# Kernel optimization log

Hardware: AMD Instinct MI355X
Metric: run time of the kernel (lower is better)

The kernel has to match this reference:

```python
import jax, jax.numpy as jnp
import numpy as np

K = 20
EPS = 1e-5


def _knn_idx(pts, k):
    # pts: [B,N,C] -> [B,N,k] indices of k nearest neighbors (self included),
    # matching torch topk on negative squared distance.
    inner = jnp.einsum('bnc,bmc->bnm', pts, pts)
    sq = jnp.sum(pts * pts, axis=-1)
    neg_dist = 2.0 * inner - sq[:, :, None] - sq[:, None, :]  # [B,N,N]
    return jax.lax.top_k(neg_dist, k)[1]


def _graph_feature(pts, k):
    # pts: [B,N,C] -> edge features [B,N,k,2C] = concat(neighbor-center, center)
    idx = _knn_idx(pts, k)                       # [B,N,k]
    nb = jax.vmap(lambda p, i: p[i])(pts, idx)   # gather: [B,N,k,C]
    ctr = jnp.broadcast_to(pts[:, :, None, :], nb.shape)
    return jnp.concatenate([nb - ctr, ctr], axis=-1)


def _bn(x, g, b, axes):
    # BatchNorm with batch statistics (torch training-mode forward)
    m = jnp.mean(x, axes, keepdims=True)
    v = jnp.var(x, axes, keepdims=True)
    return (x - m) * jax.lax.rsqrt(v + EPS) * g + b


def _edge_block(pts, W, b, g, beta):
    # EdgeConv: graph feature -> 1x1 conv (matmul over channels) -> BN -> ReLU -> max over k
    f = _graph_feature(pts, K)                       # [B,N,k,2C]
    h = jnp.einsum('bnkc,oc->bnko', f, W) + b        # 1x1 conv
    h = jax.nn.relu(_bn(h, g, beta, (0, 1, 2)))
    return jnp.max(h, axis=2)                        # [B,N,O]


def _forward(x, conv1_w, conv1_b, bn1_g, bn1_b, conv2_w, conv2_b, bn2_g, bn2_b,
             conv3_w, conv3_b, bn3_g, bn3_b, conv4_w, conv4_b, bn4_g, bn4_b,
             fc1_w, fc1_b, bnf1_g, bnf1_b, fc2_w, fc2_b, bnf2_g, bnf2_b,
             fc3_w, fc3_b, bnf3_g, bnf3_b, fc4_w, fc4_b):
    pts = x[:, 0]  # squeeze(1): [B,N,3] (channels-last == torch [B,3,N] transposed)
    x1 = _edge_block(pts, conv1_w, conv1_b, bn1_g, bn1_b)   # [B,N,64]
    x2 = _edge_block(x1, conv2_w, conv2_b, bn2_g, bn2_b)    # [B,N,64]
    x3 = _edge_block(x2, conv3_w, conv3_b, bn3_g, bn3_b)    # [B,N,128]
    x4 = _edge_block(x3, conv4_w, conv4_b, bn4_g, bn4_b)    # [B,N,256]
    # maxpool over all N points (kernel (crop_point_num,1))
    x_64 = jnp.max(x2, axis=1)    # [B,64]
    x_128 = jnp.max(x3, axis=1)   # [B,128]
    x_256 = jnp.max(x4, axis=1)   # [B,256]
    h = jnp.concatenate([x_256, x_128, x_64], axis=1)  # [B,448]
    h = jax.nn.relu(_bn(h @ fc1_w.T + fc1_b, bnf1_g, bnf1_b, (0,)))
    h = jax.nn.relu(_bn(h @ fc2_w.T + fc2_b, bnf2_g, bnf2_b, (0,)))
    h = jax.nn.relu(_bn(h @ fc3_w.T + fc3_b, bnf3_g, bnf3_b, (0,)))
    return h @ fc4_w.T + fc4_b    # [B,1]


def setup_inputs() -> dict:
    key = jax.random.key(0)
    ks = jax.random.split(key, 16)
    B, N = 8, 2048
    f32 = jnp.float32

    def w(k, shape):
        return jax.random.normal(k, shape, f32) / np.float32(np.sqrt(shape[-1]))

    def bn_params(c):
        return jnp.ones((c,), f32), jnp.zeros((c,), f32)

    bn1_g, bn1_b = bn_params(64)
    bn2_g, bn2_b = bn_params(64)
    bn3_g, bn3_b = bn_params(128)
    bn4_g, bn4_b = bn_params(256)
    bnf1_g, bnf1_b = bn_params(256)
    bnf2_g, bnf2_b = bn_params(128)
    bnf3_g, bnf3_b = bn_params(16)
    return {
        'x': jax.random.normal(ks[0], (B, 1, N, 3), f32),
        'conv1_w': w(ks[1], (64, 6)),   'conv1_b': jnp.zeros((64,), f32),
        'bn1_g': bn1_g, 'bn1_b': bn1_b,
        'conv2_w': w(ks[2], (64, 128)), 'conv2_b': jnp.zeros((64,), f32),
        'bn2_g': bn2_g, 'bn2_b': bn2_b,
        'conv3_w': w(ks[3], (128, 128)), 'conv3_b': jnp.zeros((128,), f32),
        'bn3_g': bn3_g, 'bn3_b': bn3_b,
        'conv4_w': w(ks[4], (256, 256)), 'conv4_b': jnp.zeros((256,), f32),
        'bn4_g': bn4_g, 'bn4_b': bn4_b,
        'fc1_w': w(ks[5], (256, 448)), 'fc1_b': jnp.zeros((256,), f32),
        'bnf1_g': bnf1_g, 'bnf1_b': bnf1_b,
        'fc2_w': w(ks[6], (128, 256)), 'fc2_b': jnp.zeros((128,), f32),
        'bnf2_g': bnf2_g, 'bnf2_b': bnf2_b,
        'fc3_w': w(ks[7], (16, 128)), 'fc3_b': jnp.zeros((16,), f32),
        'bnf3_g': bnf3_g, 'bnf3_b': bnf3_b,
        'fc4_w': w(ks[8], (1, 16)), 'fc4_b': jnp.zeros((1,), f32),
    }


def reference(x, conv1_w, conv1_b, bn1_g, bn1_b, conv2_w, conv2_b, bn2_g, bn2_b,
              conv3_w, conv3_b, bn3_g, bn3_b, conv4_w, conv4_b, bn4_g, bn4_b,
              fc1_w, fc1_b, bnf1_g, bnf1_b, fc2_w, fc2_b, bnf2_g, bnf2_b,
              fc3_w, fc3_b, bnf3_g, bnf3_b, fc4_w, fc4_b):
    return _forward(x, conv1_w, conv1_b, bn1_g, bn1_b, conv2_w, conv2_b, bn2_g, bn2_b,
                    conv3_w, conv3_b, bn3_g, bn3_b, conv4_w, conv4_b, bn4_g, bn4_b,
                    fc1_w, fc1_b, bnf1_g, bnf1_b, fc2_w, fc2_b, bnf2_g, bnf2_b,
                    fc3_w, fc3_b, bnf3_g, bnf3_b, fc4_w, fc4_b)
```

## Files before the change

kernel.cpp:

```cpp
#include <hip/hip_runtime.h>
#include <hip/hip_bf16.h>
#include <cfloat>

constexpr int BATCH = 8, NPTS = 2048, KNN = 20;
constexpr int NROWS = BATCH * NPTS;
constexpr float EPSV = 1e-5f;
constexpr int QCAP = 512;
constexpr int SB = 256;
constexpr int PR = 64;
constexpr int RBB = NPTS / 16;

using u16 = unsigned short;
using u64 = unsigned long long;
typedef __attribute__((ext_vector_type(8))) short short8;
typedef __attribute__((ext_vector_type(4))) float f32x4;

__global__ void diag_kernel(float* out, float v) {
    if (threadIdx.x < 8) out[threadIdx.x] = v;
}

__global__ __launch_bounds__(256) void fill_zero_kernel(float* __restrict__ p, int n) {
    int i = blockIdx.x * 256 + threadIdx.x;
    if (i < n) p[i] = 0.f;
}

template<int C>
__global__ __launch_bounds__(256) void sqnorm_kernel(const float* __restrict__ X,
                                                     float* __restrict__ sq) {
    int r = blockIdx.x * 256 + threadIdx.x;
    const float* x = X + (size_t)r * C;
    float s = 0.f;
#pragma unroll
    for (int c = 0; c < C; ++c) { float v = x[c]; s = fmaf(v, v, s); }
    sq[r] = s;
}

template<int C>
__global__ __launch_bounds__(256) void split_pack_kernel(const float* __restrict__ X,
                                                         u16* __restrict__ XPH,
                                                         u16* __restrict__ XPL) {
    constexpr int KB = C / 32;
    int e = blockIdx.x * 256 + threadIdx.x;
    int lane = e & 63;
    int rest = e >> 6;
    int kb = rest % KB;
    int Rb = rest / KB;
    int row = Rb * 16 + (lane & 15);
    int col = kb * 32 + (lane >> 4) * 8;
    const float* src = &X[(size_t)row * C + col];
    u16 h[8], l[8];
#pragma unroll
    for (int q = 0; q < 8; ++q) {
        float v = src[q];
        __hip_bfloat16 hb = __float2bfloat16(v);
        float hf = __bfloat162float(hb);
        __hip_bfloat16 lb = __float2bfloat16(v - hf);
        h[q] = *(u16*)&hb; l[q] = *(u16*)&lb;
    }
    u16* dh = &XPH[(size_t)e * 8];
    u16* dl = &XPL[(size_t)e * 8];
#pragma unroll
    for (int q = 0; q < 8; ++q) { dh[q] = h[q]; dl[q] = l[q]; }
}

template<int C, int O>
__global__ __launch_bounds__(256) void wsplit_pack_kernel(const float* __restrict__ W,
                                                          u16* __restrict__ WPH,
                                                          u16* __restrict__ WPL) {
    constexpr int KB = C / 32;
    constexpr int NFRAG = (2 * O / 16) * KB * 64;
    int e = blockIdx.x * 256 + threadIdx.x;
    if (e >= NFRAG) return;
    int lane = e & 63;
    int rest = e >> 6;
    int kb = rest % KB;
    int Nb = rest / KB;
    int n = Nb * 16 + (lane & 15);
    int col = kb * 32 + (lane >> 4) * 8;
    u16 h[8], l[8];
#pragma unroll
    for (int q = 0; q < 8; ++q) {
        int c = col + q;
        float wv = (n < O) ? W[(size_t)n * (2 * C) + c]
                           : W[(size_t)(n - O) * (2 * C) + C + c] - W[(size_t)(n - O) * (2 * C) + c];
        __hip_bfloat16 hb = __float2bfloat16(wv);
        float hf = __bfloat162float(hb);
        __hip_bfloat16 lb = __float2bfloat16(wv - hf);
        h[q] = *(u16*)&hb; l[q] = *(u16*)&lb;
    }
    u16* dh = &WPH[(size_t)e * 8];
    u16* dl = &WPL[(size_t)e * 8];
#pragma unroll
    for (int q = 0; q < 8; ++q) { dh[q] = h[q]; dl[q] = l[q]; }
}

template<int C>
__global__ __launch_bounds__(256) void dist_mfma_kernel(const u16* __restrict__ XPH,
                                                        const u16* __restrict__ XPL,
                                                        float* __restrict__ D, int b0) {
    constexpr int KB = C / 32;
    int b = b0 + blockIdx.z;
    int i0 = blockIdx.y * 64, j0 = blockIdx.x * 64;
    int w = threadIdx.x >> 6, lane = threadIdx.x & 63;
    int l15 = lane & 15, g = lane >> 4;
    size_t base = (size_t)b * RBB * KB * 512;
    int Rba = i0 / 16 + w;
    short8 ahi[KB], alo[KB];
#pragma unroll
    for (int kb = 0; kb < KB; ++kb) {
        size_t ia = base + ((size_t)(Rba * KB + kb) * 64 + lane) * 8;
        ahi[kb] = *(const short8*)&XPH[ia];
        alo[kb] = *(const short8*)&XPL[ia];
    }
    float* Dz = D + (size_t)blockIdx.z * NPTS * NPTS;
#pragma unroll
    for (int nt = 0; nt < 4; ++nt) {
        int Rbb = j0 / 16 + nt;
        f32x4 acc = {0.f, 0.f, 0.f, 0.f};
#pragma unroll
        for (int kb = 0; kb < KB; ++kb) {
            size_t ib = base + ((size_t)(Rbb * KB + kb) * 64 + lane) * 8;
            short8 bhi = *(const short8*)&XPH[ib];
            short8 blo = *(const short8*)&XPL[ib];
            acc = __builtin_amdgcn_mfma_f32_16x16x32_bf16(ahi[kb], bhi, acc, 0, 0, 0);
            acc = __builtin_amdgcn_mfma_f32_16x16x32_bf16(ahi[kb], blo, acc, 0, 0, 0);
            acc = __builtin_amdgcn_mfma_f32_16x16x32_bf16(alo[kb], bhi, acc, 0, 0, 0);
        }
        int col = j0 + nt * 16 + l15;
        int rbase = i0 + w * 16 + g * 4;
#pragma unroll
        for (int r = 0; r < 4; ++r)
            Dz[(size_t)(rbase + r) * NPTS + col] = acc[r];
    }
}

template<int C>
__global__ __launch_bounds__(256) void dist_gemm_kernel(const float* __restrict__ X,
                                                        float* __restrict__ D, int b0) {
    constexpr int KC = (C < 32) ? C : 32;
    __shared__ __align__(16) float As[KC][68];
    __shared__ __align__(16) float Bs[KC][68];
    int b = b0 + blockIdx.z;
    int i0 = blockIdx.y * 64, j0 = blockIdx.x * 64;
    const float* Xb = X + (size_t)b * NPTS * C;
    int tx = threadIdx.x & 15, ty = threadIdx.x >> 4;
    float acc[4][4] = {};
    for (int c0 = 0; c0 < C; c0 += KC) {
        for (int t = threadIdx.x; t < 64 * KC; t += 256) {
            int i = t / KC, c = t % KC;
            As[c][i] = Xb[(size_t)(i0 + i) * C + c0 + c];
            Bs[c][i] = Xb[(size_t)(j0 + i) * C + c0 + c];
        }
        __syncthreads();
#pragma unroll
        for (int c = 0; c < KC; ++c) {
            const float4 av = *(const float4*)&As[c][ty * 4];
            const float4 bv = *(const float4*)&Bs[c][tx * 4];
            float ar[4] = {av.x, av.y, av.z, av.w};
            float br[4] = {bv.x, bv.y, bv.z, bv.w};
#pragma unroll
            for (int r = 0; r < 4; ++r)
#pragma unroll
                for (int q = 0; q < 4; ++q) acc[r][q] = fmaf(ar[r], br[q], acc[r][q]);
        }
        __syncthreads();
    }
    float* Dz = D + (size_t)blockIdx.z * NPTS * NPTS;
#pragma unroll
    for (int r = 0; r < 4; ++r) {
        float4 o4 = make_float4(acc[r][0], acc[r][1], acc[r][2], acc[r][3]);
        *(float4*)&Dz[(size_t)(i0 + ty * 4 + r) * NPTS + j0 + tx * 4] = o4;
    }
}

__device__ __forceinline__ float bitonic64_desc_f32(float key, int lane) {
#pragma unroll
    for (int k = 2; k <= 64; k <<= 1) {
#pragma unroll
        for (int j = k >> 1; j > 0; j >>= 1) {
            float p = __shfl_xor(key, j);
            bool keepMax = (((lane & j) == 0) == ((lane & k) == 0));
            key = ((key > p) == keepMax) ? key : p;
        }
    }
    return key;
}

__device__ __forceinline__ u64 bitonic64_desc_u64(u64 key, int lane) {
#pragma unroll
    for (int k = 2; k <= 64; k <<= 1) {
#pragma unroll
        for (int j = k >> 1; j > 0; j >>= 1) {
            u64 p = __shfl_xor(key, j);
            bool keepMax = (((lane & j) == 0) == ((lane & k) == 0));
            key = ((key > p) == keepMax) ? key : p;
        }
    }
    return key;
}

__global__ __launch_bounds__(256) void topk_kernel(const float* __restrict__ D,
                                                   const float* __restrict__ sq,
                                                   u16* __restrict__ idx_out, int b0) {
    __shared__ u64 qkey[4][QCAP];
    __shared__ int qn[4];
    int b = b0 + blockIdx.z;
    int w = threadIdx.x >> 6, lane = threadIdx.x & 63;
    int i = blockIdx.x * 4 + w;
    const float* Drow = D + ((size_t)blockIdx.z * NPTS + i) * NPTS;
    const float* sqb = sq + b * NPTS;
    float sqi = sqb[i];
    if (lane == 0) qn[w] = 0;

    float vals[32];
    float mx = -FLT_MAX;
#pragma unroll
    for (int t = 0; t < 8; ++t) {
        int j = t * 256 + lane * 4;
        float4 v4 = *(const float4*)&Drow[j];
        float4 s4 = *(const float4*)&sqb[j];
        float a0 = (2.f * v4.x - sqi - s4.x) + 0.f;
        float a1 = (2.f * v4.y - sqi - s4.y) + 0.f;
        float a2 = (2.f * v4.z - sqi - s4.z) + 0.f;
        float a3 = (2.f * v4.w - sqi - s4.w) + 0.f;
        vals[t * 4 + 0] = a0; vals[t * 4 + 1] = a1;
        vals[t * 4 + 2] = a2; vals[t * 4 + 3] = a3;
        mx = fmaxf(mx, fmaxf(fmaxf(a0, a1), fmaxf(a2, a3)));
    }

    float sm = bitonic64_desc_f32(mx, lane);
    float T0 = __shfl(sm, 19);

#pragma unroll
    for (int t = 0; t < 32; ++t) {
        float v = vals[t];
        if (v >= T0) {
            unsigned j = (unsigned)((t >> 2) * 256 + lane * 4 + (t & 3));
            unsigned bu = __float_as_uint(v);
            unsigned u = (bu & 0x80000000u) ? ~bu : (bu | 0x80000000u);
            u64 key = ((u64)u << 32) | (u64)(0xFFFFFFFFu - j);
            int slot = atomicAdd(&qn[w], 1);
            if (slot < QCAP) qkey[w][slot] = key;
        }
    }
    int C = qn[w];
    if (C > QCAP) C = QCAP;

    u64 key = (lane < C) ? qkey[w][lane] : 0ull;
    key = bitonic64_desc_u64(key, lane);
    int base = 64;
    while (base < C) {
        if (lane >= 20) {
            int src = base + (lane - 20);
            key = (src < C) ? qkey[w][src] : 0ull;
        }
        key = bitonic64_desc_u64(key, lane);
        base += 44;
    }
    if (lane < 20) {
        unsigned j = 0xFFFFFFFFu - (unsigned)(key & 0xFFFFFFFFull);
        idx_out[(size_t)(b * NPTS + i) * KNN + lane] = (u16)j;
    }
}

template<int C, int O>
__global__ __launch_bounds__(256) void uvb_mfma_kernel(const u16* __restrict__ XPH,
                                                       const u16* __restrict__ XPL,
                                                       const u16* __restrict__ WPH,
                                                       const u16* __restrict__ WPL,
                                                       const float* __restrict__ bias,
                                                       float* __restrict__ UVA) {
    constexpr int KB = C / 32;
    int b = blockIdx.z;
    int r0 = blockIdx.y * 64, n0 = blockIdx.x * 64;
    int w = threadIdx.x >> 6, lane = threadIdx.x & 63;
    int l15 = lane & 15, g = lane >> 4;
    size_t base = (size_t)b * RBB * KB * 512;
    int Rba = r0 / 16 + w;
    short8 ahi[KB], alo[KB];
#pragma unroll
    for (int kb = 0; kb < KB; ++kb) {
        size_t ia = base + ((size_t)(Rba * KB + kb) * 64 + lane) * 8;
        ahi[kb] = *(const short8*)&XPH[ia];
        alo[kb] = *(const short8*)&XPL[ia];
    }
    float* UVb = UVA + (size_t)b * NPTS * 2 * O;
#pragma unroll
    for (int nt = 0; nt < 4; ++nt) {
        int Nb = n0 / 16 + nt;
        f32x4 acc = {0.f, 0.f, 0.f, 0.f};
#pragma unroll
        for (int kb = 0; kb < KB; ++kb) {
            size_t ib = ((size_t)(Nb * KB + kb) * 64 + lane) * 8;
            short8 bhi = *(const short8*)&WPH[ib];
            short8 blo = *(const short8*)&WPL[ib];
            acc = __builtin_amdgcn_mfma_f32_16x16x32_bf16(ahi[kb], bhi, acc, 0, 0, 0);
            acc = __builtin_amdgcn_mfma_f32_16x16x32_bf16(ahi[kb], blo, acc, 0, 0, 0);
            acc = __builtin_amdgcn_mfma_f32_16x16x32_bf16(alo[kb], bhi, acc, 0, 0, 0);
        }
        int n = n0 + nt * 16 + l15;
        float badd = (n >= O) ? bias[n - O] : 0.f;
        int rbase = r0 + w * 16 + g * 4;
#pragma unroll
        for (int r = 0; r < 4; ++r)
            UVb[(size_t)(rbase + r) * (2 * O) + n] = acc[r] + badd;
    }
}

template<int C, int O>
__global__ __launch_bounds__(256) void uvb_gemm_kernel(const float* __restrict__ X,
                                                       const float* __restrict__ W,
                                                       const float* __restrict__ bias,
                                                       float* __restrict__ UVA) {
    constexpr int KC = (C < 32) ? C : 32;
    __shared__ __align__(16) float As[KC][68];
    __shared__ __align__(16) float Bs[KC][68];
    int b = blockIdx.z;
    int r0 = blockIdx.y * 64, n0 = blockIdx.x * 64;
    int tx = threadIdx.x & 15, ty = threadIdx.x >> 4;
    float acc[4][4] = {};
    for (int c0 = 0; c0 < C; c0 += KC) {
        for (int t = threadIdx.x; t < 64 * KC; t += 256) {
            int i = t / KC, c = t % KC;
            As[c][i] = X[(size_t)(b * NPTS + r0 + i) * C + c0 + c];
            int n = n0 + i;
            float wv;
            if (n < O) wv = W[(size_t)n * (2 * C) + c0 + c];
            else {
                int o = n - O;
                wv = W[(size_t)o * (2 * C) + C + c0 + c] - W[(size_t)o * (2 * C) + c0 + c];
            }
            Bs[c][i] = wv;
        }
        __syncthreads();
#pragma unroll
        for (int c = 0; c < KC; ++c) {
            const float4 av = *(const float4*)&As[c][ty * 4];
            const float4 bv = *(const float4*)&Bs[c][tx * 4];
            float ar[4] = {av.x, av.y, av.z, av.w};
            float br[4] = {bv.x, bv.y, bv.z, bv.w};
#pragma unroll
            for (int r = 0; r < 4; ++r)
#pragma unroll
                for (int q = 0; q < 4; ++q) acc[r][q] = fmaf(ar[r], br[q], acc[r][q]);
// ... 231 lines not shown
                                                   const float* __restrict__ g3, const float* __restrict__ be3,
                                                   const float* __restrict__ w4, const float* __restrict__ b4,
                                                   float* __restrict__ out) {
    __shared__ __align__(16) float B2[128 * 8];
    __shared__ __align__(16) float C3[16 * 8];
    int tid = threadIdx.x;
    if (tid < 128) {
        int o = tid;
        float acc[8] = {};
        for (int c = 0; c < 256; ++c) {
            float wv = w2T[c * 128 + o];
            const float4 a0 = *(const float4*)&A[c * 8];
            const float4 a1 = *(const float4*)&A[c * 8 + 4];
            acc[0] = fmaf(wv, a0.x, acc[0]); acc[1] = fmaf(wv, a0.y, acc[1]);
            acc[2] = fmaf(wv, a0.z, acc[2]); acc[3] = fmaf(wv, a0.w, acc[3]);
            acc[4] = fmaf(wv, a1.x, acc[4]); acc[5] = fmaf(wv, a1.y, acc[5]);
            acc[6] = fmaf(wv, a1.z, acc[6]); acc[7] = fmaf(wv, a1.w, acc[7]);
        }
        float bb = b2[o];
        float h[8], m = 0.f;
#pragma unroll
        for (int b = 0; b < 8; ++b) { h[b] = acc[b] + bb; m += h[b]; }
        m *= 0.125f;
        float var = 0.f;
#pragma unroll
        for (int b = 0; b < 8; ++b) { float d = h[b] - m; var = fmaf(d, d, var); }
        var *= 0.125f;
        float sc = g2[o] / sqrtf(var + EPSV);
        float t = be2[o] - m * sc;
#pragma unroll
        for (int b = 0; b < 8; ++b) B2[o * 8 + b] = fmaxf(fmaf(sc, h[b], t), 0.f);
    }
    __syncthreads();
    if (tid < 16) {
        int o = tid;
        float acc[8] = {};
        for (int c = 0; c < 128; ++c) {
            float wv = w3T[c * 16 + o];
            const float4 a0 = *(const float4*)&B2[c * 8];
            const float4 a1 = *(const float4*)&B2[c * 8 + 4];
            acc[0] = fmaf(wv, a0.x, acc[0]); acc[1] = fmaf(wv, a0.y, acc[1]);
            acc[2] = fmaf(wv, a0.z, acc[2]); acc[3] = fmaf(wv, a0.w, acc[3]);
            acc[4] = fmaf(wv, a1.x, acc[4]); acc[5] = fmaf(wv, a1.y, acc[5]);
            acc[6] = fmaf(wv, a1.z, acc[6]); acc[7] = fmaf(wv, a1.w, acc[7]);
        }
        float bb = b3[o];
        float h[8], m = 0.f;
#pragma unroll
        for (int b = 0; b < 8; ++b) { h[b] = acc[b] + bb; m += h[b]; }
        m *= 0.125f;
        float var = 0.f;
#pragma unroll
        for (int b = 0; b < 8; ++b) { float d = h[b] - m; var = fmaf(d, d, var); }
        var *= 0.125f;
        float sc = g3[o] / sqrtf(var + EPSV);
        float t = be3[o] - m * sc;
#pragma unroll
        for (int b = 0; b < 8; ++b) C3[o * 8 + b] = fmaxf(fmaf(sc, h[b], t), 0.f);
    }
    __syncthreads();
    if (tid < 8) {
        int b = tid;
        float acc = b4[0];
#pragma unroll
        for (int c = 0; c < 16; ++c) acc = fmaf(w4[c], C3[c * 8 + b], acc);
        out[b] = acc;
    }
}

struct Arena {
    char* base; size_t off, cap; bool ok;
    Arena(void* b, size_t c) : base((char*)b), off(0), cap(c), ok(true) {}
    void* get(size_t bytes) {
        char* p = base + off;
        off += (bytes + 255) & ~(size_t)255;
        if (off > cap) ok = false;
        return p;
    }
};

template<int C, int O>
static void run_stage(const float* Xin, float* Xout, const float* W, const float* bias,
                      const float* g, const float* be, float* SCRBIG, float* UVA,
                      u16* XPH, u16* XPL, u16* WPH, u16* WPL,
                      u16* IDX, float* SQ, float* PART, float* PART2, float* BNP, hipStream_t s) {
    dim3 blk(256);
    float* HMAX = SCRBIG;
    float* HMIN = SCRBIG + (size_t)NROWS * O;
    sqnorm_kernel<C><<<NROWS / 256, blk, 0, s>>>(Xin, SQ);
    if constexpr (C >= 32) {
        split_pack_kernel<C><<<NROWS * C / 8 / 256, blk, 0, s>>>(Xin, XPH, XPL);
        for (int b0 = 0; b0 < BATCH; b0 += 4) {
            dist_mfma_kernel<C><<<dim3(NPTS / 64, NPTS / 64, 4), blk, 0, s>>>(XPH, XPL, SCRBIG, b0);
            topk_kernel<<<dim3(NPTS / 4, 1, 4), blk, 0, s>>>(SCRBIG, SQ, IDX, b0);
        }
        wsplit_pack_kernel<C, O><<<(2 * O * C / 8 + 255) / 256, blk, 0, s>>>(W, WPH, WPL);
        uvb_mfma_kernel<C, O><<<dim3(2 * O / 64, NPTS / 64, BATCH), blk, 0, s>>>(XPH, XPL, WPH, WPL, bias, UVA);
    } else {
        for (int b0 = 0; b0 < BATCH; b0 += 4) {
            dist_gemm_kernel<C><<<dim3(NPTS / 64, NPTS / 64, 4), blk, 0, s>>>(Xin, SCRBIG, b0);
            topk_kernel<<<dim3(NPTS / 4, 1, 4), blk, 0, s>>>(SCRBIG, SQ, IDX, b0);
        }
        uvb_gemm_kernel<C, O><<<dim3(2 * O / 64, NPTS / 64, BATCH), blk, 0, s>>>(Xin, W, bias, UVA);
    }
    statsb_kernel<O><<<dim3(SB, 1, BATCH), blk, 0, s>>>(UVA, IDX, PART, HMAX, HMIN);
    part_reduce_kernel<O><<<PR, blk, 0, s>>>(PART, PART2);
    bnp_kernel<O><<<1, O, 0, s>>>(PART2, g, be, BNP);
    applyb_kernel<O><<<NROWS * (O / 4) / 256, blk, 0, s>>>(HMAX, HMIN, BNP, Xout);
}

static void run_stage4(const float* Xin, const float* W, const float* bias,
                       const float* g, const float* be, float* SCRBIG, float* UVA,
                       u16* XPH, u16* XPL, u16* WPH, u16* WPL,
                       u16* IDX, float* SQ, float* PART, float* PART2, float* BNP, float* G0T,
                       hipStream_t s) {
    constexpr int C = 128;
    dim3 blk(256);
    float* HMAX = SCRBIG;
    float* HMIN = SCRBIG + (size_t)NROWS * 256;
    sqnorm_kernel<C><<<NROWS / 256, blk, 0, s>>>(Xin, SQ);
    split_pack_kernel<C><<<NROWS * C / 8 / 256, blk, 0, s>>>(Xin, XPH, XPL);
    for (int b0 = 0; b0 < BATCH; b0 += 4) {
        dist_mfma_kernel<C><<<dim3(NPTS / 64, NPTS / 64, 4), blk, 0, s>>>(XPH, XPL, SCRBIG, b0);
        topk_kernel<<<dim3(NPTS / 4, 1, 4), blk, 0, s>>>(SCRBIG, SQ, IDX, b0);
    }
    wsplit_pack_kernel<C, 256><<<(512 * C / 8 + 255) / 256, blk, 0, s>>>(W, WPH, WPL);
    uvb_mfma_kernel<C, 256><<<dim3(8, NPTS / 64, BATCH), blk, 0, s>>>(XPH, XPL, WPH, WPL, bias, UVA);
    statsb_kernel<256><<<dim3(SB, 1, BATCH), blk, 0, s>>>(UVA, IDX, PART, HMAX, HMIN);
    part_reduce_kernel<256><<<PR, blk, 0, s>>>(PART, PART2);
    bnp_kernel<256><<<1, 256, 0, s>>>(PART2, g, be, BNP);
    fill_zero_kernel<<<14, blk, 0, s>>>(G0T, 448 * 8);
    applyb4_kernel<<<dim3(32, 1, BATCH), blk, 0, s>>>(HMAX, HMIN, BNP, G0T);
}

extern "C" void kernel_launch(void* const* d_in, const int* in_sizes, int n_in,
                              void* d_out, int out_size, void* d_ws, size_t ws_size,
                              hipStream_t stream) {
    float* out = (float*)d_out;
    if (n_in < 31) { diag_kernel<<<1, 64, 0, stream>>>(out, 9000.f); return; }

    const float* x       = (const float*)d_in[0];
    const float* cw[4]   = {(const float*)d_in[1], (const float*)d_in[5], (const float*)d_in[9],  (const float*)d_in[13]};
    const float* cb[4]   = {(const float*)d_in[2], (const float*)d_in[6], (const float*)d_in[10], (const float*)d_in[14]};
    const float* bg[4]   = {(const float*)d_in[3], (const float*)d_in[7], (const float*)d_in[11], (const float*)d_in[15]};
    const float* bb[4]   = {(const float*)d_in[4], (const float*)d_in[8], (const float*)d_in[12], (const float*)d_in[16]};
    const float* fc1_w = (const float*)d_in[17]; const float* fc1_b = (const float*)d_in[18];
    const float* bnf1_g = (const float*)d_in[19]; const float* bnf1_b = (const float*)d_in[20];
    const float* fc2_w = (const float*)d_in[21]; const float* fc2_b = (const float*)d_in[22];
    const float* bnf2_g = (const float*)d_in[23]; const float* bnf2_b = (const float*)d_in[24];
    const float* fc3_w = (const float*)d_in[25]; const float* fc3_b = (const float*)d_in[26];
    const float* bnf3_g = (const float*)d_in[27]; const float* bnf3_b = (const float*)d_in[28];
    const float* fc4_w = (const float*)d_in[29]; const float* fc4_b = (const float*)d_in[30];

    Arena ar(d_ws, ws_size);
    float* X1 = (float*)ar.get((size_t)NROWS * 64 * 4);
    float* X2 = (float*)ar.get((size_t)NROWS * 64 * 4);
    float* X3 = (float*)ar.get((size_t)NROWS * 128 * 4);
    u16* IDX = (u16*)ar.get((size_t)NROWS * KNN * 2);
    float* SQ = (float*)ar.get((size_t)NROWS * 4);
    float* PART = (float*)ar.get((size_t)BATCH * SB * 512 * 4);
    float* PART2 = (float*)ar.get((size_t)PR * 512 * 4);
    float* BNP = (float*)ar.get(512 * 4);
    float* G0T = (float*)ar.get(448 * 8 * 4);
    float* ABUF = (float*)ar.get(256 * 8 * 4);
    u16* XPH = (u16*)ar.get((size_t)NROWS * 128 * 2);
    u16* XPL = (u16*)ar.get((size_t)NROWS * 128 * 2);
    u16* WPH = (u16*)ar.get(512 * 128 * 2);
    u16* WPL = (u16*)ar.get(512 * 128 * 2);
    float* SCRBIG = (float*)ar.get((size_t)4 * NPTS * NPTS * 4);
    if (!ar.ok) {
        diag_kernel<<<1, 64, 0, stream>>>(out, 3000.f + (float)(ws_size >> 20));
        return;
    }
    float* UVA = SCRBIG + (size_t)2 * NPTS * NPTS;

    dim3 blk(256);
    run_stage<3, 64>(x, X1, cw[0], cb[0], bg[0], bb[0], SCRBIG, UVA, XPH, XPL, WPH, WPL, IDX, SQ, PART, PART2, BNP, stream);
    run_stage<64, 64>(X1, X2, cw[1], cb[1], bg[1], bb[1], SCRBIG, UVA, XPH, XPL, WPH, WPL, IDX, SQ, PART, PART2, BNP, stream);
    run_stage<64, 128>(X2, X3, cw[2], cb[2], bg[2], bb[2], SCRBIG, UVA, XPH, XPL, WPH, WPL, IDX, SQ, PART, PART2, BNP, stream);
    run_stage4(X3, cw[3], cb[3], bg[3], bb[3], SCRBIG, UVA, XPH, XPL, WPH, WPL, IDX, SQ, PART, PART2, BNP, G0T, stream);

    gmax23_kernel<<<dim3(BATCH, 64), blk, 0, stream>>>(X2, X3, G0T);

    float* W1T = SCRBIG;
    float* W2T = W1T + 448 * 256;
    float* W3T = W2T + 256 * 128;
    transpose_kernel<<<(256 * 448 + 255) / 256, blk, 0, stream>>>(fc1_w, W1T, 256, 448);
    transpose_kernel<<<(128 * 256 + 255) / 256, blk, 0, stream>>>(fc2_w, W2T, 128, 256);
    transpose_kernel<<<(16 * 128 + 255) / 256, blk, 0, stream>>>(fc3_w, W3T, 16, 128);
    fc1_kernel<<<4, 64, 0, stream>>>(G0T, W1T, fc1_b, bnf1_g, bnf1_b, ABUF);
    tail_kernel<<<1, 256, 0, stream>>>(ABUF, W2T, fc2_b, bnf2_g, bnf2_b,
                                       W3T, fc3_b, bnf3_g, bnf3_b, fc4_w, fc4_b, out);
}
```

Measured before the change: 682.7 us.

## Fuse distance GEMM with top-k selection using threshold pass and candidate merge

The separate distance-matrix MFMA kernel and top-k kernel are replaced by a fused knn_kernel. It recomputes each row's distances over two 1024-column chunks in two passes. Pass one takes column-group maxima and uses their 20th largest value as a threshold. Pass two collects into shared memory only the candidates at or above that threshold, sorts them, and a small merge kernel combines the two chunks' top-20 lists. This removes writing and rereading the full N×N distance matrix for each stage, at the cost of doubling the MFMA work and leaving only 512 blocks. The candidate buffer is capped at 64 per row, so many ties at the threshold could silently drop valid neighbors.

```diff
diff --git a/kernel.cpp b/kernel.cpp
--- a/kernel.cpp
+++ b/kernel.cpp
@@ -5,10 +5,11 @@
 constexpr int BATCH = 8, NPTS = 2048, KNN = 20;
 constexpr int NROWS = BATCH * NPTS;
 constexpr float EPSV = 1e-5f;
-constexpr int QCAP = 512;
 constexpr int SB = 256;
 constexpr int PR = 64;
 constexpr int RBB = NPTS / 16;
+constexpr int KCAP = 64;
+constexpr int QCAP = 512;
 
 using u16 = unsigned short;
 using u64 = unsigned long long;
@@ -94,44 +95,30 @@
     for (int q = 0; q < 8; ++q) { dh[q] = h[q]; dl[q] = l[q]; }
 }
 
-template<int C>
-__global__ __launch_bounds__(256) void dist_mfma_kernel(const u16* __restrict__ XPH,
-                                                        const u16* __restrict__ XPL,
-                                                        float* __restrict__ D, int b0) {
-    constexpr int KB = C / 32;
-    int b = b0 + blockIdx.z;
-    int i0 = blockIdx.y * 64, j0 = blockIdx.x * 64;
-    int w = threadIdx.x >> 6, lane = threadIdx.x & 63;
-    int l15 = lane & 15, g = lane >> 4;
-    size_t base = (size_t)b * RBB * KB * 512;
-    int Rba = i0 / 16 + w;
-    short8 ahi[KB], alo[KB];
-#pragma unroll
-    for (int kb = 0; kb < KB; ++kb) {
-        size_t ia = base + ((size_t)(Rba * KB + kb) * 64 + lane) * 8;
-        ahi[kb] = *(const short8*)&XPH[ia];
-        alo[kb] = *(const short8*)&XPL[ia];
-    }
-    float* Dz = D + (size_t)blockIdx.z * NPTS * NPTS;
-#pragma unroll
-    for (int nt = 0; nt < 4; ++nt) {
-        int Rbb = j0 / 16 + nt;
-        f32x4 acc = {0.f, 0.f, 0.f, 0.f};
-#pragma unroll
-        for (int kb = 0; kb < KB; ++kb) {
-            size_t ib = base + ((size_t)(Rbb * KB + kb) * 64 + lane) * 8;
-            short8 bhi = *(const short8*)&XPH[ib];
-            short8 blo = *(const short8*)&XPL[ib];
-            acc = __builtin_amdgcn_mfma_f32_16x16x32_bf16(ahi[kb], bhi, acc, 0, 0, 0);
-            acc = __builtin_amdgcn_mfma_f32_16x16x32_bf16(ahi[kb], blo, acc, 0, 0, 0);
-            acc = __builtin_amdgcn_mfma_f32_16x16x32_bf16(alo[kb], bhi, acc, 0, 0, 0);
-        }
-        int col = j0 + nt * 16 + l15;
-        int rbase = i0 + w * 16 + g * 4;
-#pragma unroll
-        for (int r = 0; r < 4; ++r)
-            Dz[(size_t)(rbase + r) * NPTS + col] = acc[r];
-    }
+__device__ __forceinline__ float bitonic64_desc_f32(float key, int lane) {
+#pragma unroll
+    for (int k = 2; k <= 64; k <<= 1) {
+#pragma unroll
+        for (int j = k >> 1; j > 0; j >>= 1) {
+            float p = __shfl_xor(key, j);
+            bool keepMax = (((lane & j) == 0) == ((lane & k) == 0));
+            key = ((key > p) == keepMax) ? key : p;
+        }
+    }
+    return key;
+}
+
+__device__ __forceinline__ u64 bitonic64_desc_u64(u64 key, int lane) {
+#pragma unroll
+    for (int k = 2; k <= 64; k <<= 1) {
+#pragma unroll
+        for (int j = k >> 1; j > 0; j >>= 1) {
+            u64 p = __shfl_xor(key, j);
+            bool keepMax = (((lane & j) == 0) == ((lane & k) == 0));
+            key = ((key > p) == keepMax) ? key : p;
+        }
+    }
+    return key;
 }
 
 template<int C>
@@ -173,32 +160,6 @@
     }
 }
 
-__device__ __forceinline__ float bitonic64_desc_f32(float key, int lane) {
-#pragma unroll
-    for (int k = 2; k <= 64; k <<= 1) {
-#pragma unroll
-        for (int j = k >> 1; j > 0; j >>= 1) {
-            float p = __shfl_xor(key, j);
-            bool keepMax = (((lane & j) == 0) == ((lane & k) == 0));
-            key = ((key > p) == keepMax) ? key : p;
-        }
-    }
-    return key;
-}
-
-__device__ __forceinline__ u64 bitonic64_desc_u64(u64 key, int lane) {
-#pragma unroll
-    for (int k = 2; k <= 64; k <<= 1) {
-#pragma unroll
-        for (int j = k >> 1; j > 0; j >>= 1) {
-            u64 p = __shfl_xor(key, j);
-            bool keepMax = (((lane & j) == 0) == ((lane & k) == 0));
-            key = ((key > p) == keepMax) ? key : p;
-        }
-    }
-    return key;
-}
-
 __global__ __launch_bounds__(256) void topk_kernel(const float* __restrict__ D,
                                                    const float* __restrict__ sq,
                                                    u16* __restrict__ idx_out, int b0) {
@@ -260,6 +221,138 @@
     if (lane < 20) {
         unsigned j = 0xFFFFFFFFu - (unsigned)(key & 0xFFFFFFFFull);
         idx_out[(size_t)(b * NPTS + i) * KNN + lane] = (u16)j;
+    }
+}
+
+template<int C>
+__global__ __launch_bounds__(256) void knn_kernel(const u16* __restrict__ XPH,
+                                                  const u16* __restrict__ XPL,
+                                                  const float* __restrict__ SQ,
+                                                  u64* __restrict__ CAND) {
+    constexpr int KB = C / 32;
+    __shared__ float cmax[64][65];
+    __shared__ u64 cand[64][KCAP];
+    __shared__ float Ts[64];
+    __shared__ int cnt[64];
+    int b = blockIdx.z;
+    int chunk = blockIdx.x;
+    int i0 = blockIdx.y * 64;
+    int w = threadIdx.x >> 6, lane = threadIdx.x & 63;
+    int l15 = lane & 15, g = lane >> 4;
+    size_t base = (size_t)b * RBB * KB * 512;
+    const float* sqb = SQ + b * NPTS;
+
+    int Rba = i0 / 16 + w;
+    short8 ahi[KB], alo[KB];
+#pragma unroll
+    for (int kb = 0; kb < KB; ++kb) {
+        size_t ia = base + ((size_t)(Rba * KB + kb) * 64 + lane) * 8;
+        ahi[kb] = *(const short8*)&XPH[ia];
+        alo[kb] = *(const short8*)&XPL[ia];
+    }
+    int rbase = i0 + w * 16 + g * 4;
+    float sqr[4];
+#pragma unroll
+    for (int r = 0; r < 4; ++r) sqr[r] = sqb[rbase + r];
+
+    float rm[4][4];
+#pragma unroll
+    for (int r = 0; r < 4; ++r)
+#pragma unroll
+        for (int nt = 0; nt < 4; ++nt) rm[r][nt] = -FLT_MAX;
+    for (int jt = 0; jt < 16; ++jt) {
+        int j0 = chunk * 1024 + jt * 64;
+#pragma unroll
+        for (int nt = 0; nt < 4; ++nt) {
+            int Rbb = j0 / 16 + nt;
+            f32x4 acc = {0.f, 0.f, 0.f, 0.f};
+#pragma unroll
+            for (int kb = 0; kb < KB; ++kb) {
+                size_t ib = base + ((size_t)(Rbb * KB + kb) * 64 + lane) * 8;
+                short8 bhi = *(const short8*)&XPH[ib];
+                short8 blo = *(const short8*)&XPL[ib];
+                acc = __builtin_amdgcn_mfma_f32_16x16x32_bf16(ahi[kb], bhi, acc, 0, 0, 0);
+                acc = __builtin_amdgcn_mfma_f32_16x16x32_bf16(ahi[kb], blo, acc, 0, 0, 0);
+                acc = __builtin_amdgcn_mfma_f32_16x16x32_bf16(alo[kb], bhi, acc, 0, 0, 0);
+            }
+            int col = j0 + nt * 16 + l15;
+            float sqc = sqb[col];
+#pragma unroll
+            for (int r = 0; r < 4; ++r) {
+                float v = (2.f * acc[r] - sqr[r] - sqc) + 0.f;
+                rm[r][nt] = fmaxf(rm[r][nt], v);
+            }
+        }
+    }
+    int rowloc0 = w * 16 + g * 4;
+#pragma unroll
+    for (int r = 0; r < 4; ++r)
+#pragma unroll
+        for (int nt = 0; nt < 4; ++nt)
+            cmax[rowloc0 + r][l15 * 4 + nt] = rm[r][nt];
+    if (threadIdx.x < 64) cnt[threadIdx.x] = 0;
+    __syncthreads();
+    for (int rr = 0; rr < 16; ++rr) {
+        int row = w * 16 + rr;
+        float sv = bitonic64_desc_f32(cmax[row][lane], lane);
+        if (lane == 19) Ts[row] = sv;
+    }
+    __syncthreads();
+
+    for (int jt = 0; jt < 16; ++jt) {
+        int j0 = chunk * 1024 + jt * 64;
+#pragma unroll
+        for (int nt = 0; nt < 4; ++nt) {
+            int Rbb = j0 / 16 + nt;
+            f32x4 acc = {0.f, 0.f, 0.f, 0.f};
+#pragma unroll
+            for (int kb = 0; kb < KB; ++kb) {
+                size_t ib = base + ((size_t)(Rbb * KB + kb) * 64 + lane) * 8;
+                short8 bhi = *(const short8*)&XPH[ib];
+                short8 blo = *(const short8*)&XPL[ib];
+                acc = __builtin_amdgcn_mfma_f32_16x16x32_bf16(ahi[kb], bhi, acc, 0, 0, 0);
+                acc = __builtin_amdgcn_mfma_f32_16x16x32_bf16(ahi[kb], blo, acc, 0, 0, 0);
+                acc = __builtin_amdgcn_mfma_f32_16x16x32_bf16(alo[kb], bhi, acc, 0, 0, 0);
+            }
+            int col = j0 + nt * 16 + l15;
+            float sqc = sqb[col];
+#pragma unroll
+            for (int r = 0; r < 4; ++r) {
+                float v = (2.f * acc[r] - sqr[r] - sqc) + 0.f;
+                int rowloc = rowloc0 + r;
+                if (v >= Ts[rowloc]) {
+                    unsigned bu = __float_as_uint(v);
+                    unsigned u = (bu & 0x80000000u) ? ~bu : (bu | 0x80000000u);
+                    u64 key = ((u64)u << 32) | (u64)(0xFFFFFFFFu - (unsigned)col);
+                    int slot = atomicAdd(&cnt[rowloc], 1);
+                    if (slot < KCAP) cand[rowloc][slot] = key;
+                }
+            }
+        }
+    }
+    __syncthreads();
+
+    for (int rr = 0; rr < 16; ++rr) {
+        int row = w * 16 + rr;
+        int Cn = cnt[row]; if (Cn > KCAP) Cn = KCAP;
+        u64 key = (lane < Cn) ? cand[row][lane] : 0ull;
+        key = bitonic64_desc_u64(key, lane);
+        if (lane < 20)
+            CAND[(((size_t)(b * NPTS + i0 + row)) * 2 + chunk) * 20 + lane] = key;
+    }
+}
+
+__global__ __launch_bounds__(256) void knn_merge_kernel(const u64* __restrict__ CAND,
+                                                        u16* __restrict__ idx_out) {
+    int b = blockIdx.z;
+    int w = threadIdx.x >> 6, lane = threadIdx.x & 63;
+    int i = blockIdx.x * 4 + w;
+    size_t rb = ((size_t)(b * NPTS + i)) * 40;
+    u64 key = (lane < 40) ? CAND[rb + lane] : 0ull;
+    key = bitonic64_desc_u64(key, lane);
+    if (lane < 20) {
+        unsigned j = 0xFFFFFFFFu - (unsigned)(key & 0xFFFFFFFFull);
+        idx_out[((size_t)(b * NPTS + i)) * KNN + lane] = (u16)j;
     }
 }
 
@@ -657,7 +750,7 @@
 template<int C, int O>
 static void run_stage(const float* Xin, float* Xout, const float* W, const float* bias,
                       const float* g, const float* be, float* SCRBIG, float* UVA,
-                      u16* XPH, u16* XPL, u16* WPH, u16* WPL,
+                      u16* XPH, u16* XPL, u16* WPH, u16* WPL, u64* CANDB,
                       u16* IDX, float* SQ, float* PART, float* PART2, float* BNP, hipStream_t s) {
     dim3 blk(256);
     float* HMAX = SCRBIG;
@@ -665,10 +758,8 @@
     sqnorm_kernel<C><<<NROWS / 256, blk, 0, s>>>(Xin, SQ);
     if constexpr (C >= 32) {
         split_pack_kernel<C><<<NROWS * C / 8 / 256, blk, 0, s>>>(Xin, XPH, XPL);
-        for (int b0 = 0; b0 < BATCH; b0 += 4) {
-            dist_mfma_kernel<C><<<dim3(NPTS / 64, NPTS / 64, 4), blk, 0, s>>>(XPH, XPL, SCRBIG, b0);
-            topk_kernel<<<dim3(NPTS / 4, 1, 4), blk, 0, s>>>(SCRBIG, SQ, IDX, b0);
-        }
+        knn_kernel<C><<<dim3(2, NPTS / 64, BATCH), blk, 0, s>>>(XPH, XPL, SQ, CANDB);
+        knn_merge_kernel<<<dim3(NPTS / 4, 1, BATCH), blk, 0, s>>>(CANDB, IDX);
         wsplit_pack_kernel<C, O><<<(2 * O * C / 8 + 255) / 256, blk, 0, s>>>(W, WPH, WPL);
         uvb_mfma_kernel<C, O><<<dim3(2 * O / 64, NPTS / 64, BATCH), blk, 0, s>>>(XPH, XPL, WPH, WPL, bias, UVA);
     } else {
@@ -686,7 +777,7 @@
 
 static void run_stage4(const float* Xin, const float* W, const float* bias,
                        const float* g, const float* be, float* SCRBIG, float* UVA,
-                       u16* XPH, u16* XPL, u16* WPH, u16* WPL,
+                       u16* XPH, u16* XPL, u16* WPH, u16* WPL, u64* CANDB,
                        u16* IDX, float* SQ, float* PART, float* PART2, float* BNP, float* G0T,
                        hipStream_t s) {
     constexpr int C = 128;
@@ -695,10 +786,8 @@
     float* HMIN = SCRBIG + (size_t)NROWS * 256;
     sqnorm_kernel<C><<<NROWS / 256, blk, 0, s>>>(Xin, SQ);
     split_pack_kernel<C><<<NROWS * C / 8 / 256, blk, 0, s>>>(Xin, XPH, XPL);
-    for (int b0 = 0; b0 < BATCH; b0 += 4) {
-        dist_mfma_kernel<C><<<dim3(NPTS / 64, NPTS / 64, 4), blk, 0, s>>>(XPH, XPL, SCRBIG, b0);
-        topk_kernel<<<dim3(NPTS / 4, 1, 4), blk, 0, s>>>(SCRBIG, SQ, IDX, b0);
-    }
+    knn_kernel<C><<<dim3(2, NPTS / 64, BATCH), blk, 0, s>>>(XPH, XPL, SQ, CANDB);
+    knn_merge_kernel<<<dim3(NPTS / 4, 1, BATCH), blk, 0, s>>>(CANDB, IDX);
     wsplit_pack_kernel<C, 256><<<(512 * C / 8 + 255) / 256, blk, 0, s>>>(W, WPH, WPL);
     uvb_mfma_kernel<C, 256><<<dim3(8, NPTS / 64, BATCH), blk, 0, s>>>(XPH, XPL, WPH, WPL, bias, UVA);
     statsb_kernel<256><<<dim3(SB, 1, BATCH), blk, 0, s>>>(UVA, IDX, PART, HMAX, HMIN);
@@ -742,6 +831,7 @@
     u16* XPL = (u16*)ar.get((size_t)NROWS * 128 * 2);
     u16* WPH = (u16*)ar.get(512 * 128 * 2);
     u16* WPL = (u16*)ar.get(512 * 128 * 2);
+    u64* CANDB = (u64*)ar.get((size_t)NROWS * 40 * 8);
     float* SCRBIG = (float*)ar.get((size_t)4 * NPTS * NPTS * 4);
     if (!ar.ok) {
         diag_kernel<<<1, 64, 0, stream>>>(out, 3000.f + (float)(ws_size >> 20));
@@ -750,10 +840,10 @@
     float* UVA = SCRBIG + (size_t)2 * NPTS * NPTS;
 
     dim3 blk(256);
-    run_stage<3, 64>(x, X1, cw[0], cb[0], bg[0], bb[0], SCRBIG, UVA, XPH, XPL, WPH, WPL, IDX, SQ, PART, PART2, BNP, stream);
-    run_stage<64, 64>(X1, X2, cw[1], cb[1], bg[1], bb[1], SCRBIG, UVA, XPH, XPL, WPH, WPL, IDX, SQ, PART, PART2, BNP, stream);
-    run_stage<64, 128>(X2, X3, cw[2], cb[2], bg[2], bb[2], SCRBIG, UVA, XPH, XPL, WPH, WPL, IDX, SQ, PART, PART2, BNP, stream);
-    run_stage4(X3, cw[3], cb[3], bg[3], bb[3], SCRBIG, UVA, XPH, XPL, WPH, WPL, IDX, SQ, PART, PART2, BNP, G0T, stream);
+    run_stage<3, 64>(x, X1, cw[0], cb[0], bg[0], bb[0], SCRBIG, UVA, XPH, XPL, WPH, WPL, CANDB, IDX, SQ, PART, PART2, BNP, stream);
+    run_stage<64, 64>(X1, X2, cw[1], cb[1], bg[1], bb[1], SCRBIG, UVA, XPH, XPL, WPH, WPL, CANDB, IDX, SQ, PART, PART2, BNP, stream);
+    run_stage<64, 128>(X2, X3, cw[2], cb[2], bg[2], bb[2], SCRBIG, UVA, XPH, XPL, WPH, WPL, CANDB, IDX, SQ, PART, PART2, BNP, stream);
+    run_stage4(X3, cw[3], cb[3], bg[3], bb[3], SCRBIG, UVA, XPH, XPL, WPH, WPL, CANDB, IDX, SQ, PART, PART2, BNP, G0T, stream);
 
     gmax23_kernel<<<dim3(BATCH, 64), blk, 0, stream>>>(X2, X3, G0T);
 
```

Measured after the change: 868.9 us. 1.27x slower.

## Fuse MFMA distance computation with chunked top-k selection for kNN

Applied to the files above, without the earlier changes.

Replaces the separate distance GEMM, which wrote a full NxN distance matrix to global memory, and the row-wise top-k kernel with a fused kNN kernel. Each block computes distances for 16 rows against a 512-column chunk in LDS and selects per-chunk top-20 candidates with a threshold and bitonic sort. A small merge kernel then combines the four chunk candidate lists. This removes the large global round trip of the distance matrix for stages with C>=32. The per-chunk candidate buffer is capped at 48, which risks dropping candidates when many values tie.

```diff
diff --git a/kernel.cpp b/kernel.cpp
--- a/kernel.cpp
+++ b/kernel.cpp
@@ -5,10 +5,12 @@
 constexpr int BATCH = 8, NPTS = 2048, KNN = 20;
 constexpr int NROWS = BATCH * NPTS;
 constexpr float EPSV = 1e-5f;
-constexpr int QCAP = 512;
 constexpr int SB = 256;
 constexpr int PR = 64;
 constexpr int RBB = NPTS / 16;
+constexpr int KC2 = 48;
+constexpr int QCAP = 512;
+constexpr int NCH = 4;
 
 using u16 = unsigned short;
 using u64 = unsigned long long;
@@ -94,44 +96,30 @@
     for (int q = 0; q < 8; ++q) { dh[q] = h[q]; dl[q] = l[q]; }
 }
 
-template<int C>
-__global__ __launch_bounds__(256) void dist_mfma_kernel(const u16* __restrict__ XPH,
-                                                        const u16* __restrict__ XPL,
-                                                        float* __restrict__ D, int b0) {
-    constexpr int KB = C / 32;
-    int b = b0 + blockIdx.z;
-    int i0 = blockIdx.y * 64, j0 = blockIdx.x * 64;
-    int w = threadIdx.x >> 6, lane = threadIdx.x & 63;
-    int l15 = lane & 15, g = lane >> 4;
-    size_t base = (size_t)b * RBB * KB * 512;
-    int Rba = i0 / 16 + w;
-    short8 ahi[KB], alo[KB];
-#pragma unroll
-    for (int kb = 0; kb < KB; ++kb) {
-        size_t ia = base + ((size_t)(Rba * KB + kb) * 64 + lane) * 8;
-        ahi[kb] = *(const short8*)&XPH[ia];
-        alo[kb] = *(const short8*)&XPL[ia];
-    }
-    float* Dz = D + (size_t)blockIdx.z * NPTS * NPTS;
-#pragma unroll
-    for (int nt = 0; nt < 4; ++nt) {
-        int Rbb = j0 / 16 + nt;
-        f32x4 acc = {0.f, 0.f, 0.f, 0.f};
-#pragma unroll
-        for (int kb = 0; kb < KB; ++kb) {
-            size_t ib = base + ((size_t)(Rbb * KB + kb) * 64 + lane) * 8;
-            short8 bhi = *(const short8*)&XPH[ib];
-            short8 blo = *(const short8*)&XPL[ib];
-            acc = __builtin_amdgcn_mfma_f32_16x16x32_bf16(ahi[kb], bhi, acc, 0, 0, 0);
-            acc = __builtin_amdgcn_mfma_f32_16x16x32_bf16(ahi[kb], blo, acc, 0, 0, 0);
-            acc = __builtin_amdgcn_mfma_f32_16x16x32_bf16(alo[kb], bhi, acc, 0, 0, 0);
-        }
-        int col = j0 + nt * 16 + l15;
-        int rbase = i0 + w * 16 + g * 4;
-#pragma unroll
-        for (int r = 0; r < 4; ++r)
-            Dz[(size_t)(rbase + r) * NPTS + col] = acc[r];
-    }
+__device__ __forceinline__ float bitonic64_desc_f32(float key, int lane) {
+#pragma unroll
+    for (int k = 2; k <= 64; k <<= 1) {
+#pragma unroll
+        for (int j = k >> 1; j > 0; j >>= 1) {
+            float p = __shfl_xor(key, j);
+            bool keepMax = (((lane & j) == 0) == ((lane & k) == 0));
+            key = ((key > p) == keepMax) ? key : p;
+        }
+    }
+    return key;
+}
+
+__device__ __forceinline__ u64 bitonic64_desc_u64(u64 key, int lane) {
+#pragma unroll
+    for (int k = 2; k <= 64; k <<= 1) {
+#pragma unroll
+        for (int j = k >> 1; j > 0; j >>= 1) {
+            u64 p = __shfl_xor(key, j);
+            bool keepMax = (((lane & j) == 0) == ((lane & k) == 0));
+            key = ((key > p) == keepMax) ? key : p;
+        }
+    }
+    return key;
 }
 
 template<int C>
@@ -173,32 +161,6 @@
     }
 }
 
-__device__ __forceinline__ float bitonic64_desc_f32(float key, int lane) {
-#pragma unroll
-    for (int k = 2; k <= 64; k <<= 1) {
-#pragma unroll
-        for (int j = k >> 1; j > 0; j >>= 1) {
-            float p = __shfl_xor(key, j);
-            bool keepMax = (((lane & j) == 0) == ((lane & k) == 0));
-            key = ((key > p) == keepMax) ? key : p;
-        }
-    }
-    return key;
-}
-
-__device__ __forceinline__ u64 bitonic64_desc_u64(u64 key, int lane) {
-#pragma unroll
-    for (int k = 2; k <= 64; k <<= 1) {
-#pragma unroll
-        for (int j = k >> 1; j > 0; j >>= 1) {
-            u64 p = __shfl_xor(key, j);
-            bool keepMax = (((lane & j) == 0) == ((lane & k) == 0));
-            key = ((key > p) == keepMax) ? key : p;
-        }
-    }
-    return key;
-}
-
 __global__ __launch_bounds__(256) void topk_kernel(const float* __restrict__ D,
                                                    const float* __restrict__ sq,
                                                    u16* __restrict__ idx_out, int b0) {
@@ -260,6 +222,108 @@
     if (lane < 20) {
         unsigned j = 0xFFFFFFFFu - (unsigned)(key & 0xFFFFFFFFull);
         idx_out[(size_t)(b * NPTS + i) * KNN + lane] = (u16)j;
+    }
+}
+
+template<int C>
+__global__ __launch_bounds__(256) void knn_kernel(const u16* __restrict__ XPH,
+                                                  const u16* __restrict__ XPL,
+                                                  const float* __restrict__ SQ,
+                                                  u64* __restrict__ CAND) {
+    constexpr int KB = C / 32;
+    __shared__ float Dl[16][516];
+    __shared__ u64 cand[16][KC2];
+    __shared__ int cnt[16];
+    int b = blockIdx.z;
+    int chunk = blockIdx.x;
+    int i0 = blockIdx.y * 16;
+    int w = threadIdx.x >> 6, lane = threadIdx.x & 63;
+    int l15 = lane & 15, g = lane >> 4;
+    size_t base = (size_t)b * RBB * KB * 512;
+    const float* sqb = SQ + b * NPTS;
+
+    if (threadIdx.x < 16) cnt[threadIdx.x] = 0;
+
+    int Rba = i0 / 16;
+    short8 ahi[KB], alo[KB];
+#pragma unroll
+    for (int kb = 0; kb < KB; ++kb) {
+        size_t ia = base + ((size_t)(Rba * KB + kb) * 64 + lane) * 8;
+        ahi[kb] = *(const short8*)&XPH[ia];
+        alo[kb] = *(const short8*)&XPL[ia];
+    }
+    float sqr[4];
+#pragma unroll
+    for (int r = 0; r < 4; ++r) sqr[r] = sqb[i0 + g * 4 + r];
+
+#pragma unroll
+    for (int t = 0; t < 8; ++t) {
+        int c = w + 4 * t;
+        int Cb = chunk * 32 + c;
+        f32x4 acc = {0.f, 0.f, 0.f, 0.f};
+#pragma unroll
+        for (int kb = 0; kb < KB; ++kb) {
+            size_t ib = base + ((size_t)(Cb * KB + kb) * 64 + lane) * 8;
+            short8 bhi = *(const short8*)&XPH[ib];
+            short8 blo = *(const short8*)&XPL[ib];
+            acc = __builtin_amdgcn_mfma_f32_16x16x32_bf16(ahi[kb], bhi, acc, 0, 0, 0);
+            acc = __builtin_amdgcn_mfma_f32_16x16x32_bf16(ahi[kb], blo, acc, 0, 0, 0);
+            acc = __builtin_amdgcn_mfma_f32_16x16x32_bf16(alo[kb], bhi, acc, 0, 0, 0);
+        }
+        int colg = Cb * 16 + l15;
+        float sqc = sqb[colg];
+        int cl = c * 16 + l15;
+#pragma unroll
+        for (int r = 0; r < 4; ++r)
+            Dl[g * 4 + r][cl] = (2.f * acc[r] - sqr[r] - sqc) + 0.f;
+    }
+    __syncthreads();
+
+    for (int rr = 0; rr < 4; ++rr) {
+        int row = w * 4 + rr;
+        float vv[8];
+        float mx = -FLT_MAX;
+#pragma unroll
+        for (int q = 0; q < 8; ++q) {
+            vv[q] = Dl[row][lane + 64 * q];
+            mx = fmaxf(mx, vv[q]);
+        }
+        float sv = bitonic64_desc_f32(mx, lane);
+        float T = __shfl(sv, 19);
+#pragma unroll
+        for (int q = 0; q < 8; ++q) {
+            float v = vv[q];
+            if (v >= T) {
+                unsigned colg = (unsigned)(chunk * 512 + lane + 64 * q);
+                unsigned bu = __float_as_uint(v);
+                unsigned u = (bu & 0x80000000u) ? ~bu : (bu | 0x80000000u);
+                u64 key = ((u64)u << 32) | (u64)(0xFFFFFFFFu - colg);
+                int slot = atomicAdd(&cnt[row], 1);
+                if (slot < KC2) cand[row][slot] = key;
+            }
+        }
+        int Cn = cnt[row]; if (Cn > KC2) Cn = KC2;
+        u64 key = (lane < Cn) ? cand[row][lane] : 0ull;
+        key = bitonic64_desc_u64(key, lane);
+        if (lane < 20)
+            CAND[(((size_t)(b * NPTS + i0 + row)) * NCH + chunk) * 20 + lane] = key;
+    }
+}
+
+__global__ __launch_bounds__(256) void knn_merge_kernel(const u64* __restrict__ CAND,
+                                                        u16* __restrict__ idx_out) {
+    int b = blockIdx.z;
+    int w = threadIdx.x >> 6, lane = threadIdx.x & 63;
+    int i = blockIdx.x * 4 + w;
+    size_t rb = ((size_t)(b * NPTS + i)) * (NCH * 20);
+    u64 key = CAND[rb + lane];
+    key = bitonic64_desc_u64(key, lane);
+    u64 extra = (lane >= 20 && lane < 36) ? CAND[rb + 64 + (lane - 20)] : 0ull;
+    if (lane >= 20) key = extra;
+    key = bitonic64_desc_u64(key, lane);
+    if (lane < 20) {
+        unsigned j = 0xFFFFFFFFu - (unsigned)(key & 0xFFFFFFFFull);
+        idx_out[((size_t)(b * NPTS + i)) * KNN + lane] = (u16)j;
     }
 }
 
@@ -662,13 +726,12 @@
     dim3 blk(256);
     float* HMAX = SCRBIG;
     float* HMIN = SCRBIG + (size_t)NROWS * O;
+    u64* CANDB = (u64*)SCRBIG;
     sqnorm_kernel<C><<<NROWS / 256, blk, 0, s>>>(Xin, SQ);
     if constexpr (C >= 32) {
         split_pack_kernel<C><<<NROWS * C / 8 / 256, blk, 0, s>>>(Xin, XPH, XPL);
-        for (int b0 = 0; b0 < BATCH; b0 += 4) {
-            dist_mfma_kernel<C><<<dim3(NPTS / 64, NPTS / 64, 4), blk, 0, s>>>(XPH, XPL, SCRBIG, b0);
-            topk_kernel<<<dim3(NPTS / 4, 1, 4), blk, 0, s>>>(SCRBIG, SQ, IDX, b0);
-        }
+        knn_kernel<C><<<dim3(NCH, NPTS / 16, BATCH), blk, 0, s>>>(XPH, XPL, SQ, CANDB);
+        knn_merge_kernel<<<dim3(NPTS / 4, 1, BATCH), blk, 0, s>>>(CANDB, IDX);
         wsplit_pack_kernel<C, O><<<(2 * O * C / 8 + 255) / 256, blk, 0, s>>>(W, WPH, WPL);
         uvb_mfma_kernel<C, O><<<dim3(2 * O / 64, NPTS / 64, BATCH), blk, 0, s>>>(XPH, XPL, WPH, WPL, bias, UVA);
     } else {
@@ -693,12 +756,11 @@
     dim3 blk(256);
     float* HMAX = SCRBIG;
     float* HMIN = SCRBIG + (size_t)NROWS * 256;
+    u64* CANDB = (u64*)SCRBIG;
     sqnorm_kernel<C><<<NROWS / 256, blk, 0, s>>>(Xin, SQ);
     split_pack_kernel<C><<<NROWS * C / 8 / 256, blk, 0, s>>>(Xin, XPH, XPL);
-    for (int b0 = 0; b0 < BATCH; b0 += 4) {
-        dist_mfma_kernel<C><<<dim3(NPTS / 64, NPTS / 64, 4), blk, 0, s>>>(XPH, XPL, SCRBIG, b0);
-        topk_kernel<<<dim3(NPTS / 4, 1, 4), blk, 0, s>>>(SCRBIG, SQ, IDX, b0);
-    }
+    knn_kernel<C><<<dim3(NCH, NPTS / 16, BATCH), blk, 0, s>>>(XPH, XPL, SQ, CANDB);
+    knn_merge_kernel<<<dim3(NPTS / 4, 1, BATCH), blk, 0, s>>>(CANDB, IDX);
     wsplit_pack_kernel<C, 256><<<(512 * C / 8 + 255) / 256, blk, 0, s>>>(W, WPH, WPL);
     uvb_mfma_kernel<C, 256><<<dim3(8, NPTS / 64, BATCH), blk, 0, s>>>(XPH, XPL, WPH, WPL, bias, UVA);
     statsb_kernel<256><<<dim3(SB, 1, BATCH), blk, 0, s>>>(UVA, IDX, PART, HMAX, HMIN);
```

Measured after the change: 718.2 us. 5.2% more time.
